# Optimization experiments

Measured on AMD Instinct MI355X. Metric: run time of the kernel, lower is better.

## Reference

```python
import jax, jax.numpy as jnp
import numpy as np

B, N, D = 4, 1024, 1024
H, DH = 16, 64            # heads, dim_head; inner_dim = H*DH = D
CTX_N, CTX_D = 77, 768    # CLIP text context
FF_IN, FF_HID = 8 * D, 4 * D  # GEGLU: proj to 2*4*D, gate to 4*D
EPS = 1e-5
SCALE = DH ** -0.5
NL = 256                  # 2**8 levels for all quantizers
ZP_QKV = 128.0            # asymmetric 8-bit zero point for q/k/v
ZP_W = 0.0                # always_zero=True for softmax-weight quantizer


def _round_ste(t):
    return t + jax.lax.stop_gradient(jnp.round(t) - t)


def _fake_quant(x, delta, zp):
    xq = jnp.clip(_round_ste(x / delta) + zp, 0.0, NL - 1.0)
    return (xq - zp) * delta


def _ln(x, w, b):
    m = x.mean(-1, keepdims=True)
    v = x.var(-1, keepdims=True)
    return (x - m) * jax.lax.rsqrt(v + EPS) * w + b


def _split_heads(t):  # [b, n, h*d] -> [b, h, n, d]
    b, n, _ = t.shape
    return t.reshape(b, n, H, DH).transpose(0, 2, 1, 3)


def _attn(x, ctx, wq, wk, wv, wo, bo, dq, dk, dv, dw):
    q = _split_heads(x @ wq)
    k = _split_heads(ctx @ wk)
    v = _split_heads(ctx @ wv)
    qq = _fake_quant(q, dq, ZP_QKV)
    kk = _fake_quant(k, dk, ZP_QKV)
    sim = jnp.einsum('bhid,bhjd->bhij', qq, kk) * SCALE
    attn = jax.nn.softmax(sim, axis=-1)
    aw = _fake_quant(attn, dw, ZP_W)
    vv = _fake_quant(v, dv, ZP_QKV)
    out = jnp.einsum('bhij,bhjd->bhid', aw, vv)
    b, _, n, _ = out.shape
    out = out.transpose(0, 2, 1, 3).reshape(b, n, H * DH)
    return out @ wo + bo


def _geglu_ff(x, w1, b1, w2, b2):
    h = x @ w1 + b1
    a, g = jnp.split(h, 2, axis=-1)
    return (a * jax.nn.gelu(g, approximate=False)) @ w2 + b2


def setup_inputs() -> dict:
    key = jax.random.key(0)
    ks = jax.random.split(key, 16)
    w = lambda i, shp, s: jax.random.normal(ks[i], shp, jnp.float32) * s
    sD = D ** -0.5
    sC = CTX_D ** -0.5
    return {
        'x': jax.random.normal(ks[0], (B, N, D), jnp.float32),
        'context': jax.random.normal(ks[1], (B, CTX_N, CTX_D), jnp.float32),
        'norm1_w': jnp.ones((D,), jnp.float32), 'norm1_b': jnp.zeros((D,), jnp.float32),
        'norm2_w': jnp.ones((D,), jnp.float32), 'norm2_b': jnp.zeros((D,), jnp.float32),
        'norm3_w': jnp.ones((D,), jnp.float32), 'norm3_b': jnp.zeros((D,), jnp.float32),
        'a1_wq': w(2, (D, D), sD), 'a1_wk': w(3, (D, D), sD), 'a1_wv': w(4, (D, D), sD),
        'a1_wo': w(5, (D, D), sD), 'a1_bo': jnp.zeros((D,), jnp.float32),
        'a2_wq': w(6, (D, D), sD), 'a2_wk': w(7, (CTX_D, D), sC), 'a2_wv': w(8, (CTX_D, D), sC),
        'a2_wo': w(9, (D, D), sD), 'a2_bo': jnp.zeros((D,), jnp.float32),
        'ff_w1': w(10, (D, FF_IN), sD), 'ff_b1': jnp.zeros((FF_IN,), jnp.float32),
        'ff_w2': w(11, (FF_HID, D), FF_HID ** -0.5), 'ff_b2': jnp.zeros((D,), jnp.float32),
        'd1_q': jnp.asarray(0.02, jnp.float32), 'd1_k': jnp.asarray(0.02, jnp.float32),
        'd1_v': jnp.asarray(0.02, jnp.float32), 'd1_w': jnp.asarray(1.0 / 255.0, jnp.float32),
        'd2_q': jnp.asarray(0.02, jnp.float32), 'd2_k': jnp.asarray(0.02, jnp.float32),
        'd2_v': jnp.asarray(0.02, jnp.float32), 'd2_w': jnp.asarray(1.0 / 255.0, jnp.float32),
    }


def reference(x, context, norm1_w, norm1_b, norm2_w, norm2_b, norm3_w, norm3_b,
              a1_wq, a1_wk, a1_wv, a1_wo, a1_bo,
              a2_wq, a2_wk, a2_wv, a2_wo, a2_bo,
              ff_w1, ff_b1, ff_w2, ff_b2,
              d1_q, d1_k, d1_v, d1_w, d2_q, d2_k, d2_v, d2_w):
    # attn1: quantized self-attention
    x = _attn(_ln(x, norm1_w, norm1_b), _ln(x, norm1_w, norm1_b),
              a1_wq, a1_wk, a1_wv, a1_wo, a1_bo, d1_q, d1_k, d1_v, d1_w) + x
    # attn2: quantized cross-attention with text context
    x = _attn(_ln(x, norm2_w, norm2_b), context,
              a2_wq, a2_wk, a2_wv, a2_wo, a2_bo, d2_q, d2_k, d2_v, d2_w) + x
    # GEGLU feed-forward
    x = _geglu_ff(_ln(x, norm3_w, norm3_b), ff_w1, ff_b1, ff_w2, ff_b2) + x
    return x
```

## Files before the change

kernel.cpp:

```cpp
#include <hip/hip_runtime.h>
#include <math.h>


typedef unsigned short u16;
typedef __attribute__((ext_vector_type(8))) short short8;
typedef __attribute__((ext_vector_type(4))) float f32x4;

__device__ inline float b2f(u16 v) { return __uint_as_float(((unsigned)v) << 16); }
__device__ inline u16 f2b(float f) {
  unsigned u = __float_as_uint(f);
  unsigned r = u + 0x7fffu + ((u >> 16) & 1u);
  return (u16)(r >> 16);
}

__device__ inline float exp2_fast(float x) {
#if __has_builtin(__builtin_amdgcn_exp2f)
  return __builtin_amdgcn_exp2f(x);
#else
  return __expf(x * 0.6931471805599453f);
#endif
}

__device__ inline void glds16(const u16* g, u16* l) {
  __builtin_amdgcn_global_load_lds(
      (const __attribute__((address_space(1))) void*)g,
      (__attribute__((address_space(3))) void*)l, 16, 0, 0);
}

__global__ __launch_bounds__(256) void transpose_k(const float* __restrict__ in,
                                                   u16* __restrict__ out,
                                                   int R, int C) {
  __shared__ float t[32][33];
  int tx = threadIdx.x & 31, ty = threadIdx.x >> 5;
  int c0 = blockIdx.x * 32, r0 = blockIdx.y * 32;
#pragma unroll
  for (int i = 0; i < 32; i += 8)
    t[ty + i][tx] = in[(size_t)(r0 + ty + i) * C + c0 + tx];
  __syncthreads();
#pragma unroll
  for (int i = 0; i < 32; i += 8)
    out[(size_t)(c0 + ty + i) * R + r0 + tx] = f2b(t[tx][ty + i]);
}

struct TrBatch { const float* in[4]; u16* out[4]; int R[4]; };
__global__ __launch_bounds__(256) void transpose4_k(TrBatch a) {
  int z = blockIdx.z;
  const float* in = a.in[z];
  u16* out = a.out[z];
  int R = a.R[z];
  int r0 = blockIdx.y * 32;
  if (r0 >= R) return;
  __shared__ float t[32][33];
  int tx = threadIdx.x & 31, ty = threadIdx.x >> 5;
  int c0 = blockIdx.x * 32;
#pragma unroll
  for (int i = 0; i < 32; i += 8)
    t[ty + i][tx] = in[(size_t)(r0 + ty + i) * 1024 + c0 + tx];
  __syncthreads();
#pragma unroll
  for (int i = 0; i < 32; i += 8)
    out[(size_t)(c0 + ty + i) * R + r0 + tx] = f2b(t[tx][ty + i]);
}

__global__ __launch_bounds__(256) void tr16_k(const u16* __restrict__ in,
                                              u16* __restrict__ out, int NK,
                                              int NKP) {
  __shared__ u16 t[32][33];
  int tx = threadIdx.x & 31, ty = threadIdx.x >> 5;
  int n0 = blockIdx.x * 32, c0 = blockIdx.y * 32, b = blockIdx.z;
  const u16* ib = in + (size_t)b * NK * 1024;
  u16* ob = out + (size_t)b * 1024 * NKP;
#pragma unroll
  for (int i = 0; i < 32; i += 8) {
    int n = n0 + ty + i;
    n = n < NK ? n : NK - 1;
    t[ty + i][tx] = ib[(size_t)n * 1024 + c0 + tx];
  }
  __syncthreads();
#pragma unroll
  for (int i = 0; i < 32; i += 8)
    ob[(size_t)(c0 + ty + i) * NKP + n0 + tx] = t[tx][ty + i];
}

__global__ __launch_bounds__(256) void cast_k(const float* __restrict__ in,
                                              u16* __restrict__ out) {
  int i = (blockIdx.x * 256 + threadIdx.x) * 4;
  float4 v = *(const float4*)(in + i);
  out[i + 0] = f2b(v.x);
  out[i + 1] = f2b(v.y);
  out[i + 2] = f2b(v.z);
  out[i + 3] = f2b(v.w);
}

__global__ __launch_bounds__(256) void zero_k(float4* __restrict__ out) {
  float4 z = {0.f, 0.f, 0.f, 0.f};
  out[blockIdx.x * 256 + threadIdx.x] = z;
}

__global__ __launch_bounds__(256) void ln_k(const float* __restrict__ X,
                                            const float* __restrict__ W,
                                            const float* __restrict__ Bi,
                                            u16* __restrict__ Out) {
  const int row = blockIdx.x, tid = threadIdx.x;
  float4 x = *(const float4*)(X + (size_t)row * 1024 + tid * 4);
  float s = x.x + x.y + x.z + x.w;
  float s2 = x.x * x.x + x.y * x.y + x.z * x.z + x.w * x.w;
#pragma unroll
  for (int off = 32; off >= 1; off >>= 1) {
    s += __shfl_down(s, off);
    s2 += __shfl_down(s2, off);
  }
  __shared__ float red[8];
  int wave = tid >> 6, lane = tid & 63;
  if (lane == 0) { red[wave] = s; red[4 + wave] = s2; }
  __syncthreads();
  s = red[0] + red[1] + red[2] + red[3];
  s2 = red[4] + red[5] + red[6] + red[7];
  float mean = s * 0.0009765625f;
  float var = s2 * 0.0009765625f - mean * mean;
  float rs = rsqrtf(var + 1e-5f);
  float4 w = *(const float4*)(W + tid * 4);
  float4 b = *(const float4*)(Bi + tid * 4);
  u16* orow = Out + (size_t)row * 1024 + tid * 4;
  orow[0] = f2b((x.x - mean) * rs * w.x + b.x);
  orow[1] = f2b((x.y - mean) * rs * w.y + b.y);
  orow[2] = f2b((x.z - mean) * rs * w.z + b.z);
  orow[3] = f2b((x.w - mean) * rs * w.w + b.w);
}

template <int EPI, int TM>
__global__ __launch_bounds__(256, 2) void gemm_bt(
    const u16* __restrict__ A, int lda, const u16* __restrict__ Bt, int ldb,
    void* __restrict__ Cp, int ldc, const float* __restrict__ bias,
    const float* __restrict__ res, int ldr, const float* __restrict__ dp,
    const float* __restrict__ dp2, const float* __restrict__ dp3,
    size_t segsz, int M, int N, int K) {
  __shared__ __align__(16) u16 As[TM * 64];
  __shared__ __align__(16) u16 Bs[128 * 64];
  const int tid = threadIdx.x;
  const int lane = tid & 63, wave = tid >> 6;
  const int qd = lane >> 4, cl = lane & 15;
  const int wm = (wave & 1) * (TM / 2), wn = (wave >> 1) << 6;
  const int m0 = blockIdx.x * TM, n0 = blockIdx.y * 128;

  f32x4 acc[TM / 32][4];
  const f32x4 zero = {0.f, 0.f, 0.f, 0.f};
#pragma unroll
  for (int i = 0; i < TM / 32; i++)
#pragma unroll
    for (int j = 0; j < 4; j++) acc[i][j] = zero;

  for (int k0 = 0; k0 < K; k0 += 64) {
    __syncthreads();
#pragma unroll
    for (int it = 0; it < TM / 32; ++it) {
      int ch = it * 256 + tid;
      int r = ch >> 3, cc = (ch & 7) << 3;
      int gr = m0 + r;
      gr = gr < M ? gr : M - 1;
      glds16(A + (size_t)gr * lda + k0 + cc, As + ch * 8);
    }
#pragma unroll
    for (int it = 0; it < 4; ++it) {
      int ch = it * 256 + tid;
      int r = ch >> 3, cc = (ch & 7) << 3;
      glds16(Bt + (size_t)(n0 + r) * ldb + k0 + cc, Bs + ch * 8);
    }
    __syncthreads();
#pragma unroll
    for (int ks = 0; ks < 64; ks += 32) {
      short8 af[TM / 32], bf[4];
#pragma unroll
      for (int t = 0; t < TM / 32; t++)
        af[t] = *(const short8*)(As + (wm + t * 16 + cl) * 64 + ks + qd * 8);
#pragma unroll
      for (int t = 0; t < 4; t++)
        bf[t] = *(const short8*)(Bs + (wn + t * 16 + cl) * 64 + ks + qd * 8);
#pragma unroll
      for (int mt = 0; mt < TM / 32; mt++)
#pragma unroll
        for (int nt = 0; nt < 4; nt++)
          acc[mt][nt] = __builtin_amdgcn_mfma_f32_16x16x32_bf16(
              af[mt], bf[nt], acc[mt][nt], 0, 0, 0);
    }
  }

  float dscale = 1.f;
  u16* qbase = (u16*)Cp;
  if constexpr (EPI == 0) dscale = 1.0f / dp[0];
  if constexpr (EPI == 2) {
    int seg = n0 >> 10;
    const float* ds = (seg == 0) ? dp : ((seg == 1) ? dp2 : dp3);
    dscale = 1.0f / ds[0];
    qbase = (u16*)Cp + (size_t)seg * segsz;
  }
#pragma unroll
  for (int mt = 0; mt < TM / 32; ++mt) {
#pragma unroll
    for (int r = 0; r < 4; ++r) {
      int row = m0 + wm + mt * 16 + qd * 4 + r;
      if (row >= M) continue;
#pragma unroll
      for (int nt = 0; nt < 4; ++nt) {
        int col = n0 + wn + nt * 16 + cl;
        float v = acc[mt][nt][r];
        if constexpr (EPI == 0) {
          float xq = rintf(v * dscale) + 128.f;
          xq = fminf(fmaxf(xq, 0.f), 255.f);
          qbase[(size_t)row * ldc + col] = f2b(xq - 128.f);
        } else if constexpr (EPI == 2) {
          float xq = rintf(v * dscale) + 128.f;
          xq = fminf(fmaxf(xq, 0.f), 255.f);
          qbase[(size_t)row * ldc + (col & 1023)] = f2b(xq - 128.f);
        } else {
          v += bias[col] + res[(size_t)row * ldr + col];
          ((float*)Cp)[(size_t)row * ldc + col] = v;
        }
      }
    }
  }
}

__global__ __launch_bounds__(256, 2) void gemm_bt_sk(
    const u16* __restrict__ A, int lda, const u16* __restrict__ Bt, int ldb,
    float* __restrict__ C, int ldc, const float* __restrict__ bias,
    const float* __restrict__ res, int ldr, int M, int KH) {
  __shared__ __align__(16) u16 As[128 * 64];
  __shared__ __align__(16) u16 Bs[128 * 64];
  const int tid = threadIdx.x;
  const int lane = tid & 63, wave = tid >> 6;
  const int qd = lane >> 4, cl = lane & 15;
  const int wm = (wave & 1) * 64, wn = (wave >> 1) << 6;
  const int m0 = blockIdx.x * 128, n0 = blockIdx.y * 128;
  const int kz = blockIdx.z;
  const int kbeg = kz * KH, kend = kbeg + KH;

  f32x4 acc[4][4];
  const f32x4 zero = {0.f, 0.f, 0.f, 0.f};
#pragma unroll
  for (int i = 0; i < 4; i++)
#pragma unroll
    for (int j = 0; j < 4; j++) acc[i][j] = zero;

  for (int k0 = kbeg; k0 < kend; k0 += 64) {
    __syncthreads();
#pragma unroll
    for (int it = 0; it < 4; ++it) {
      int ch = it * 256 + tid;
      int r = ch >> 3, cc = (ch & 7) << 3;
      glds16(A + (size_t)(m0 + r) * lda + k0 + cc, As + ch * 8);
    }
#pragma unroll
    for (int it = 0; it < 4; ++it) {
      int ch = it * 256 + tid;
      int r = ch >> 3, cc = (ch & 7) << 3;
      glds16(Bt + (size_t)(n0 + r) * ldb + k0 + cc, Bs + ch * 8);
    }
    __syncthreads();
#pragma unroll
    for (int ks = 0; ks < 64; ks += 32) {
      short8 af[4], bf[4];
#pragma unroll
      for (int t = 0; t < 4; t++)
        af[t] = *(const short8*)(As + (wm + t * 16 + cl) * 64 + ks + qd * 8);
#pragma unroll
      for (int t = 0; t < 4; t++)
        bf[t] = *(const short8*)(Bs + (wn + t * 16 + cl) * 64 + ks + qd * 8);
#pragma unroll
      for (int mt = 0; mt < 4; mt++)
#pragma unroll
        for (int nt = 0; nt < 4; nt++)
          acc[mt][nt] = __builtin_amdgcn_mfma_f32_16x16x32_bf16(
              af[mt], bf[nt], acc[mt][nt], 0, 0, 0);
    }
  }

#pragma unroll
  for (int mt = 0; mt < 4; ++mt) {
#pragma unroll
    for (int r = 0; r < 4; ++r) {
      int row = m0 + wm + mt * 16 + qd * 4 + r;
#pragma unroll
      for (int nt = 0; nt < 4; ++nt) {
        int col = n0 + wn + nt * 16 + cl;
        float v = acc[mt][nt][r];
        if (kz == 0) v += bias[col] + res[(size_t)row * ldr + col];
        atomicAdd(&C[(size_t)row * ldc + col], v);
      }
    }
  }
}

#define VMW(n) asm volatile("s_waitcnt vmcnt(" #n ")" ::: "memory")
#define LGKM0() asm volatile("s_waitcnt lgkmcnt(0)" ::: "memory")
#define SBAR() __builtin_amdgcn_s_barrier()
#define SCHED0() __builtin_amdgcn_sched_barrier(0)

#define ST_A(P, MH, K0)                                                      \
  do {                                                                       \
    _Pragma("unroll") for (int it = 0; it < 2; ++it) {                       \
      int r_ = (MH) * 128 + it * 64 + sr;                                    \
      glds16(Ag + (size_t)(m0 + r_) * 1024 + (K0) + ((sc ^ (r_ & 7)) << 3),  \
             As + (P) * 16384 + r_ * 64 + (sc << 3));                        \
    }                                                                        \
  } while (0)

#define ST_B(P, BH, K0)                                                      \
  do {                                                                       \
    _Pragma("unroll") for (int it = 0; it < 2; ++it) {                       \
      int r_ = it * 64 + sr;                                                 \
      glds16(W1t + (size_t)((BH) * 4096 + n0 + r_) * 1024 + (K0) +           \
                 ((sc ^ (r_ & 7)) << 3),                                     \
             Bs + (P) * 16384 + ((BH) * 128 + r_) * 64 + (sc << 3));         \
    }                                                                        \
  } while (0)

#define RDA(P, MH)                                                           \
  do {                                                                       \
    _Pragma("unroll") for (int mf = 0; mf < 4; ++mf) {                       \
      int row_ = (MH) * 128 + wr * 64 + mf * 16 + cl;                        \
      _Pragma("unroll") for (int ks = 0; ks < 2; ++ks)                       \
        af[mf * 2 + ks] = *(const short8*)(As + (P) * 16384 + row_ * 64 +    \
                                           (((ks * 4 + qd) ^ (cl & 7)) << 3)); \
    }                                                                        \
  } while (0)

#define RDB(P, NH, DST)                                                      \
  do {                                                                       \
    _Pragma("unroll") for (int nf = 0; nf < 2; ++nf) {                       \
      int j_ = (NH) * 128 + wc * 32 + nf * 16 + cl;                          \
      _Pragma("unroll") for (int ks = 0; ks < 2; ++ks)                       \
        DST[nf * 2 + ks] = *(const short8*)(Bs + (P) * 16384 + j_ * 64 +     \
                                            (((ks * 4 + qd) ^ (cl & 7)) << 3)); \
    }                                                                        \
  } while (0)

#define MFMAQ(MH, NH, BSET)                                                  \
  do {                                                                       \
    _Pragma("unroll") for (int mf = 0; mf < 4; ++mf)                         \
      _Pragma("unroll") for (int nf = 0; nf < 2; ++nf)                       \
        _Pragma("unroll") for (int ks = 0; ks < 2; ++ks)                     \
          acc[(MH) * 4 + mf][(NH) * 2 + nf] =                                \
              __builtin_amdgcn_mfma_f32_16x16x32_bf16(                       \
                  af[mf * 2 + ks], BSET[nf * 2 + ks],                        \
                  acc[(MH) * 4 + mf][(NH) * 2 + nf], 0, 0, 0);               \
  } while (0)

#define KTILE(P, KN, LAST)                                                   \
  do {                                                                       \
                            \
    RDA(P, 0);                                                               \
    RDB(P, 0, bU);                                                           \
    if (!(LAST)) ST_A((P) ^ 1, 0, KN);                                       \
    SBAR();                                                                  \
    LGKM0();                                                                 \
    SCHED0();                                                                \
    __builtin_amdgcn_s_setprio(1);                                           \
    MFMAQ(0, 0, bU);                                                         \
    __builtin_amdgcn_s_setprio(0);                                           \
    SCHED0();                                                                \
    if (LAST) { VMW(0); } else { VMW(2); }                                   \
    SBAR();                                                                  \
                                    \
    RDB(P, 1, bV);                                                           \
    if (!(LAST)) ST_B((P) ^ 1, 0, KN);                                       \
    SBAR();                                                                  \
    LGKM0();                                                                 \
    SCHED0();                                                                \
    __builtin_amdgcn_s_setprio(1);                                           \
    MFMAQ(0, 1, bV);                                                         \
    __builtin_amdgcn_s_setprio(0);                                           \
    SCHED0();                                                                \
    SBAR();                                                                  \
                                    \
    RDA(P, 1);                                                               \
    if (!(LAST)) ST_A((P) ^ 1, 1, KN);                                       \
    SBAR();                                                                  \
    LGKM0();                                                                 \
    SCHED0();                                                                \
    __builtin_amdgcn_s_setprio(1);                                           \
    MFMAQ(1, 1, bV);                                                         \
    __builtin_amdgcn_s_setprio(0);                                           \
    SCHED0();                                                                \
    SBAR();                                                                  \
                                       \
    if (!(LAST)) ST_B((P) ^ 1, 1, KN);                                       \
    SBAR();                                                                  \
    LGKM0();                                                                 \
    SCHED0();                                                                \
    __builtin_amdgcn_s_setprio(1);                                           \
    MFMAQ(1, 0, bU);                                                         \
    __builtin_amdgcn_s_setprio(0);                                           \
    SCHED0();                                                                \
    if (!(LAST)) VMW(4);                                                     \
    SBAR();                                                                  \
  } while (0)

__global__ __launch_bounds__(512, 1) void ff1_geglu8_k(
    const u16* __restrict__ Ag, const u16* __restrict__ W1t,
    const float* __restrict__ b1, u16* __restrict__ gg) {
  __shared__ __align__(16) u16 smem[65536];
  u16* As = smem;
  u16* Bs = smem + 32768;
  const int tid = threadIdx.x;
  const int lane = tid & 63, wave = tid >> 6;
  const int qd = lane >> 4, cl = lane & 15;
  const int wr = wave >> 2, wc = wave & 3;
  const int m0 = blockIdx.x * 256;
  const int n0 = blockIdx.y * 128;
  const int sr = tid >> 3, sc = tid & 7;

  f32x4 acc[8][4];
  const f32x4 zero = {0.f, 0.f, 0.f, 0.f};
#pragma unroll
  for (int i = 0; i < 8; ++i)
#pragma unroll
    for (int j = 0; j < 4; ++j) acc[i][j] = zero;
  short8 af[8], bU[4], bV[4];

  ST_A(0, 0, 0);
  ST_B(0, 0, 0);
  ST_A(0, 1, 0);
  ST_B(0, 1, 0);
  VMW(0);
  SBAR();
  SCHED0();

  int p = 0;
#pragma unroll 1
  for (int t = 0; t < 15; ++t) {
    KTILE(p, (t + 1) * 64, 0);
    p ^= 1;
  }
  KTILE(1, 0, 1);

#pragma unroll
  for (int i = 0; i < 8; ++i) {
    const int row = m0 + (i >> 2) * 128 + wr * 64 + (i & 3) * 16 + qd * 4;
#pragma unroll
    for (int nf = 0; nf < 2; ++nf) {
      const int col = n0 + wc * 32 + nf * 16 + cl;
      const float ba = b1[col];
      const float bg = b1[4096 + col];
#pragma unroll
      for (int r = 0; r < 4; ++r) {
        float a = acc[i][nf][r] + ba;
        float g = acc[i][2 + nf][r] + bg;
        float ge = 0.5f * g * (1.0f + erff(g * 0.70710678118654752f));
        gg[(size_t)(row + r) * 4096 + col] = f2b(a * ge);
      }
    }
  }
}

__global__ __launch_bounds__(256, 4) void attn_k(
    const u16* __restrict__ Q, const u16* __restrict__ Kb,
    const u16* __restrict__ VbT, u16* __restrict__ O,
    const float* dqp, const float* dkp, const float* dvp, const float* dwp,
    int NK, int NKP) {
  __shared__ __align__(16) u16 Ks[64 * 64];
  __shared__ __align__(16) u16 VTs[64 * 64];
  __shared__ __align__(16) u16 Ps[4][16 * 72];
  const int tid = threadIdx.x;
  const int lane = tid & 63, wave = tid >> 6;
  const int qd = lane >> 4, cl = lane & 15;
  const int b = blockIdx.z, h = blockIdx.y, qt = blockIdx.x;
  const float ss2 = dqp[0] * dkp[0] * 0.125f * 1.4426950408889634f;
  const float oscale = dwp[0] * dvp[0];
  const float inv_dw = 1.0f / dwp[0];
  const f32x4 zero = {0.f, 0.f, 0.f, 0.f};

  short8 qf0, qf1;
  {
    const u16* qrow =
        Q + (size_t)(b * 1024 + qt * 64 + wave * 16 + cl) * 1024 + h * 64;
    qf0 = *(const short8*)(qrow + qd * 8);
    qf1 = *(const short8*)(qrow + 32 + qd * 8);
  }

  const u16* kbase = Kb + (size_t)(b * NK) * 1024 + h * 64;
  const u16* vtbase = VbT + ((size_t)b * 1024 + h * 64) * NKP;
  const int r_st = tid >> 3;
  const int c_sw = (((tid & 7) ^ (r_st & 7)) << 3);

  float m_s = -1e30f, l_s = 0.f;
  for (int j0 = 0; j0 < NK; j0 += 64) {
    __syncthreads();
#pragma unroll
    for (int it = 0; it < 2; ++it) {
      int j = j0 + it * 32 + r_st;
      j = j < NK ? j : NK - 1;
      glds16(kbase + (size_t)j * 1024 + c_sw, Ks + (it * 256 + tid) * 8);
    }
    __syncthreads();
    const bool full = (j0 + 64 <= NK);
    float sc[16];
#pragma unroll
    for (int nt = 0; nt < 4; ++nt) {
      const int row = nt * 16 + cl, sw = cl & 7;
      short8 kf0 = *(const short8*)(Ks + row * 64 + ((qd ^ sw) << 3));
      short8 kf1 = *(const short8*)(Ks + row * 64 + (((4 | qd) ^ sw) << 3));
      f32x4 st = zero;
      st = __builtin_amdgcn_mfma_f32_16x16x32_bf16(kf0, qf0, st, 0, 0, 0);
      st = __builtin_amdgcn_mfma_f32_16x16x32_bf16(kf1, qf1, st, 0, 0, 0);
#pragma unroll
      for (int r = 0; r < 4; ++r) {
        int key = j0 + nt * 16 + qd * 4 + r;
        sc[nt * 4 + r] = (full || key < NK) ? st[r] * ss2 : -1e30f;
      }
    }
    float t0 = fmaxf(fmaxf(sc[0], sc[1]), sc[2]);
    float t1 = fmaxf(fmaxf(sc[3], sc[4]), sc[5]);
    float t2 = fmaxf(fmaxf(sc[6], sc[7]), sc[8]);
    float t3 = fmaxf(fmaxf(sc[9], sc[10]), sc[11]);
    float t4 = fmaxf(fmaxf(sc[12], sc[13]), sc[14]);
    float mx = fmaxf(fmaxf(fmaxf(t0, t1), fmaxf(t2, t3)), fmaxf(t4, sc[15]));
    mx = fmaxf(mx, __shfl_xor(mx, 16));
    mx = fmaxf(mx, __shfl_xor(mx, 32));
    float mn = fmaxf(m_s, mx);
    float ss = 0.f;
#pragma unroll
    for (int i = 0; i < 16; ++i) ss += exp2_fast(sc[i] - mn);
    ss += __shfl_xor(ss, 16);
    ss += __shfl_xor(ss, 32);
    l_s = l_s * exp2_fast(m_s - mn) + ss;
    m_s = mn;
  }
  const float mb = m_s + log2f(l_s) - log2f(inv_dw);

  f32x4 oacc[4];
#pragma unroll
  for (int t = 0; t < 4; t++) oacc[t] = zero;

  for (int j0 = 0; j0 < NK; j0 += 64) {
    __syncthreads();
#pragma unroll
    for (int it = 0; it < 2; ++it) {
      int r = it * 32 + r_st;
      int j = j0 + r;
      j = j < NK ? j : NK - 1;
      glds16(kbase + (size_t)j * 1024 + c_sw, Ks + (it * 256 + tid) * 8);
      glds16(vtbase + (size_t)r * NKP + j0 + c_sw, VTs + (it * 256 + tid) * 8);
    }
    __syncthreads();
    const bool full = (j0 + 64 <= NK);
#pragma unroll
    for (int nt = 0; nt < 4; ++nt) {
      const int row = nt * 16 + cl, sw = cl & 7;
      short8 kf0 = *(const short8*)(Ks + row * 64 + ((qd ^ sw) << 3));
      short8 kf1 = *(const short8*)(Ks + row * 64 + (((4 | qd) ^ sw) << 3));
      f32x4 st = zero;
      st = __builtin_amdgcn_mfma_f32_16x16x32_bf16(kf0, qf0, st, 0, 0, 0);
      st = __builtin_amdgcn_mfma_f32_16x16x32_bf16(kf1, qf1, st, 0, 0, 0);
      unsigned a[4];
#pragma unroll
      for (int r = 0; r < 4; ++r) {
        int key = j0 + nt * 16 + qd * 4 + r;
        float aw = 0.f;
        if (full || key < NK) {
          float e = exp2_fast(__builtin_fmaf(st[r], ss2, -mb));
          aw = fminf(rintf(e), 255.f);
        }
        a[r] = __float_as_uint(aw);
      }
      uint2 pv;
      pv.x = (a[0] >> 16) | (a[1] & 0xffff0000u);
      pv.y = (a[2] >> 16) | (a[3] & 0xffff0000u);
      *(uint2*)(&Ps[wave][cl * 72 + nt * 16 + qd * 4]) = pv;
    }
#pragma unroll
    for (int ks = 0; ks < 2; ++ks) {
      short8 pf = *(const short8*)(&Ps[wave][cl * 72 + ks * 32 + qd * 8]);
#pragma unroll
      for (int dt = 0; dt < 4; ++dt) {
        const int vrow = dt * 16 + cl;
        short8 vf = *(const short8*)(VTs + vrow * 64 +
                                     (((ks * 4 + qd) ^ (cl & 7)) << 3));
        oacc[dt] = __builtin_amdgcn_mfma_f32_16x16x32_bf16(pf, vf, oacc[dt],
                                                           0, 0, 0);
      }
    }
  }
#pragma unroll
  for (int dt = 0; dt < 4; ++dt)
#pragma unroll
    for (int r = 0; r < 4; r++) {
      size_t addr =
          (size_t)(b * 1024 + qt * 64 + wave * 16 + qd * 4 + r) * 1024 +
          h * 64 + dt * 16 + cl;
      O[addr] = f2b(oacc[dt][r] * oscale);
    }
}

extern "C" void kernel_launch(void* const* d_in, const int* in_sizes, int n_in,
                              void* d_out, int out_size, void* d_ws,
                              size_t ws_size, hipStream_t stream) {
  (void)in_sizes; (void)n_in; (void)out_size; (void)ws_size;
  const float* x    = (const float*)d_in[0];
  const float* ctx  = (const float*)d_in[1];
  const float* n1w  = (const float*)d_in[2];
  const float* n1b  = (const float*)d_in[3];
  const float* n2w  = (const float*)d_in[4];
  const float* n2b  = (const float*)d_in[5];
  const float* n3w  = (const float*)d_in[6];
  const float* n3b  = (const float*)d_in[7];
  const float* a1wq = (const float*)d_in[8];
  const float* a1wk = (const float*)d_in[9];
  const float* a1wv = (const float*)d_in[10];
  const float* a1wo = (const float*)d_in[11];
  const float* a1bo = (const float*)d_in[12];
  const float* a2wq = (const float*)d_in[13];
  const float* a2wk = (const float*)d_in[14];
  const float* a2wv = (const float*)d_in[15];
  const float* a2wo = (const float*)d_in[16];
  const float* a2bo = (const float*)d_in[17];
  const float* ffw1 = (const float*)d_in[18];
  const float* ffb1 = (const float*)d_in[19];
  const float* ffw2 = (const float*)d_in[20];
  const float* ffb2 = (const float*)d_in[21];
  const float* d1q = (const float*)d_in[22];
  const float* d1k = (const float*)d_in[23];
  const float* d1v = (const float*)d_in[24];
  const float* d1w = (const float*)d_in[25];
  const float* d2q = (const float*)d_in[26];
  const float* d2k = (const float*)d_in[27];
  const float* d2v = (const float*)d_in[28];
  const float* d2w = (const float*)d_in[29];

  char* ws = (char*)d_ws;
  const size_t MB = 1u << 20;
  u16* W    = (u16*)(ws + 0 * MB);
  u16* lnb  = (u16*)(ws + 16 * MB);
  u16* qb   = (u16*)(ws + 24 * MB);
  u16* kb   = (u16*)(ws + 32 * MB);
  u16* vb   = (u16*)(ws + 40 * MB);
  u16* vbT  = (u16*)(ws + 48 * MB);
  u16* ao   = (u16*)(ws + 56 * MB);
  float* x1 = (float*)(ws + 64 * MB);
  u16* k2b  = (u16*)(ws + 32 * MB);
  u16* v2b  = k2b + 308 * 1024;
  u16* vbTc = (u16*)(ws + 34 * MB);
  u16* ctxb = (u16*)(ws + 35 * MB);
  u16* gg   = (u16*)(ws + 24 * MB);

  u16* WT0 = W;
  u16* WT1 = (u16*)(ws + 2 * MB);
  u16* WT2 = (u16*)(ws + 4 * MB);
  u16* WT3 = (u16*)(ws + 6 * MB);
  u16* WT3c = WT2 + 1024 * 768;

  dim3 T256(256);
  {
    TrBatch tb;
    tb.in[0] = a1wq; tb.out[0] = WT0; tb.R[0] = 1024;
    tb.in[1] = a1wk; tb.out[1] = WT1; tb.R[1] = 1024;
    tb.in[2] = a1wv; tb.out[2] = WT2; tb.R[2] = 1024;
    tb.in[3] = a1wo; tb.out[3] = WT3; tb.R[3] = 1024;
    transpose4_k<<<dim3(32, 32, 4), T256, 0, stream>>>(tb);
  }
  ln_k<<<4096, T256, 0, stream>>>(x, n1w, n1b, lnb);
  gemm_bt<2, 128><<<dim3(32, 24), T256, 0, stream>>>(
      lnb, 1024, WT0, 1024, qb, 1024, nullptr, nullptr, 0, d1q, d1k, d1v,
      (size_t)4096 * 1024, 4096, 3072, 1024);
  tr16_k<<<dim3(32, 32, 4), T256, 0, stream>>>(vb, vbT, 1024, 1024);
  attn_k<<<dim3(16, 16, 4), T256, 0, stream>>>(qb, kb, vbT, ao, d1q, d1k, d1v,
                                               d1w, 1024, 1024);
  gemm_bt<1, 64><<<dim3(64, 8), T256, 0, stream>>>(
      ao, 1024, WT3, 1024, x1, 1024, a1bo, x, 1024, nullptr, nullptr, nullptr,
      0, 4096, 1024, 1024);
  {
    TrBatch tb;
    tb.in[0] = a2wq; tb.out[0] = WT0; tb.R[0] = 1024;
    tb.in[1] = a2wo; tb.out[1] = WT1; tb.R[1] = 1024;
    tb.in[2] = a2wk; tb.out[2] = WT2;  tb.R[2] = 768;
    tb.in[3] = a2wv; tb.out[3] = WT3c; tb.R[3] = 768;
    transpose4_k<<<dim3(32, 32, 4), T256, 0, stream>>>(tb);
  }
  ln_k<<<4096, T256, 0, stream>>>(x1, n2w, n2b, lnb);
  cast_k<<<231, T256, 0, stream>>>(ctx, ctxb);
  gemm_bt<0, 64><<<dim3(64, 8), T256, 0, stream>>>(
      lnb, 1024, WT0, 1024, qb, 1024, nullptr, nullptr, 0, d2q, nullptr,
      nullptr, 0, 4096, 1024, 1024);
  gemm_bt<2, 64><<<dim3(5, 16), T256, 0, stream>>>(
      ctxb, 768, WT2, 768, k2b, 1024, nullptr, nullptr, 0, d2k, d2v, nullptr,
      (size_t)308 * 1024, 308, 2048, 768);
  tr16_k<<<dim3(3, 32, 4), T256, 0, stream>>>(v2b, vbTc, 77, 128);
  attn_k<<<dim3(16, 16, 4), T256, 0, stream>>>(qb, k2b, vbTc, ao, d2q, d2k,
                                               d2v, d2w, 77, 128);
  gemm_bt<1, 64><<<dim3(64, 8), T256, 0, stream>>>(
      ao, 1024, WT1, 1024, x1, 1024, a2bo, x1, 1024, nullptr, nullptr, nullptr,
      0, 4096, 1024, 1024);
  transpose_k<<<dim3(256, 32), T256, 0, stream>>>(ffw1, W, 1024, 8192);
  ln_k<<<4096, T256, 0, stream>>>(x1, n3w, n3b, lnb);
  ff1_geglu8_k<<<dim3(16, 32), dim3(512), 0, stream>>>(lnb, W, ffb1, gg);
  transpose_k<<<dim3(32, 128), T256, 0, stream>>>(ffw2, W, 4096, 1024);
  zero_k<<<4096, T256, 0, stream>>>((float4*)d_out);
  gemm_bt_sk<<<dim3(32, 8, 2), T256, 0, stream>>>(
      gg, 4096, W, 4096, (float*)d_out, 1024, ffb2, x1, 1024, 4096, 2048);
}
```

Measured before the change: 557.0 us.

## Use 512-thread 128x128 GEMM for out-projections and FF2, drop split-K atomics

Adds a templated gemm512 kernel with 8 waves per 128x128 tile (each wave computes 64x32) and swaps it in for the two attention output projections, the cross-attention Q projection, and the FF2 GEMM. For FF2 it replaces the split-K kernel, its atomicAdd epilogue and the zero-fill launch with a single full-K pass that writes results directly. The intent is fewer launches, no atomics, and larger tiles with more waves to hide latency. The cost is fewer blocks (256) for the 1024-wide GEMMs, which may underfill the GPU, and a longer serial K loop for FF2.

```diff
diff --git a/kernel.cpp b/kernel.cpp
--- a/kernel.cpp
+++ b/kernel.cpp
@@ -90,11 +90,6 @@
   out[i + 1] = f2b(v.y);
   out[i + 2] = f2b(v.z);
   out[i + 3] = f2b(v.w);
-}
-
-__global__ __launch_bounds__(256) void zero_k(float4* __restrict__ out) {
-  float4 z = {0.f, 0.f, 0.f, 0.f};
-  out[blockIdx.x * 256 + threadIdx.x] = z;
 }
 
 __global__ __launch_bounds__(256) void ln_k(const float* __restrict__ X,
@@ -221,71 +216,79 @@
   }
 }
 
-__global__ __launch_bounds__(256, 2) void gemm_bt_sk(
+template <int EPI>
+__global__ __launch_bounds__(512, 1) void gemm512(
     const u16* __restrict__ A, int lda, const u16* __restrict__ Bt, int ldb,
-    float* __restrict__ C, int ldc, const float* __restrict__ bias,
-    const float* __restrict__ res, int ldr, int M, int KH) {
+    void* __restrict__ Cp, int ldc, const float* __restrict__ bias,
+    const float* __restrict__ res, int ldr, const float* __restrict__ dp,
+    int K) {
   __shared__ __align__(16) u16 As[128 * 64];
   __shared__ __align__(16) u16 Bs[128 * 64];
   const int tid = threadIdx.x;
   const int lane = tid & 63, wave = tid >> 6;
   const int qd = lane >> 4, cl = lane & 15;
-  const int wm = (wave & 1) * 64, wn = (wave >> 1) << 6;
+  const int wm = (wave >> 2) << 6, wn = (wave & 3) << 5;
   const int m0 = blockIdx.x * 128, n0 = blockIdx.y * 128;
-  const int kz = blockIdx.z;
-  const int kbeg = kz * KH, kend = kbeg + KH;
-
-  f32x4 acc[4][4];
+
+  f32x4 acc[4][2];
   const f32x4 zero = {0.f, 0.f, 0.f, 0.f};
 #pragma unroll
   for (int i = 0; i < 4; i++)
 #pragma unroll
-    for (int j = 0; j < 4; j++) acc[i][j] = zero;
-
-  for (int k0 = kbeg; k0 < kend; k0 += 64) {
-    __syncthreads();
-#pragma unroll
-    for (int it = 0; it < 4; ++it) {
-      int ch = it * 256 + tid;
+    for (int j = 0; j < 2; j++) acc[i][j] = zero;
+
+  for (int k0 = 0; k0 < K; k0 += 64) {
+    __syncthreads();
+#pragma unroll
+    for (int it = 0; it < 2; ++it) {
+      int ch = it * 512 + tid;
       int r = ch >> 3, cc = (ch & 7) << 3;
       glds16(A + (size_t)(m0 + r) * lda + k0 + cc, As + ch * 8);
     }
 #pragma unroll
-    for (int it = 0; it < 4; ++it) {
-      int ch = it * 256 + tid;
+    for (int it = 0; it < 2; ++it) {
+      int ch = it * 512 + tid;
       int r = ch >> 3, cc = (ch & 7) << 3;
       glds16(Bt + (size_t)(n0 + r) * ldb + k0 + cc, Bs + ch * 8);
     }
     __syncthreads();
 #pragma unroll
     for (int ks = 0; ks < 64; ks += 32) {
-      short8 af[4], bf[4];
+      short8 af[4], bf[2];
 #pragma unroll
       for (int t = 0; t < 4; t++)
         af[t] = *(const short8*)(As + (wm + t * 16 + cl) * 64 + ks + qd * 8);
 #pragma unroll
-      for (int t = 0; t < 4; t++)
+      for (int t = 0; t < 2; t++)
         bf[t] = *(const short8*)(Bs + (wn + t * 16 + cl) * 64 + ks + qd * 8);
 #pragma unroll
       for (int mt = 0; mt < 4; mt++)
 #pragma unroll
-        for (int nt = 0; nt < 4; nt++)
+        for (int nt = 0; nt < 2; nt++)
           acc[mt][nt] = __builtin_amdgcn_mfma_f32_16x16x32_bf16(
               af[mt], bf[nt], acc[mt][nt], 0, 0, 0);
     }
   }
 
+  float dscale = 1.f;
+  if constexpr (EPI == 0) dscale = 1.0f / dp[0];
 #pragma unroll
   for (int mt = 0; mt < 4; ++mt) {
 #pragma unroll
     for (int r = 0; r < 4; ++r) {
       int row = m0 + wm + mt * 16 + qd * 4 + r;
 #pragma unroll
-      for (int nt = 0; nt < 4; ++nt) {
+      for (int nt = 0; nt < 2; ++nt) {
         int col = n0 + wn + nt * 16 + cl;
         float v = acc[mt][nt][r];
-        if (kz == 0) v += bias[col] + res[(size_t)row * ldr + col];
-        atomicAdd(&C[(size_t)row * ldc + col], v);
+        if constexpr (EPI == 0) {
+          float xq = rintf(v * dscale) + 128.f;
+          xq = fminf(fmaxf(xq, 0.f), 255.f);
+          ((u16*)Cp)[(size_t)row * ldc + col] = f2b(xq - 128.f);
+        } else {
+          v += bias[col] + res[(size_t)row * ldr + col];
+          ((float*)Cp)[(size_t)row * ldc + col] = v;
+        }
       }
     }
   }
@@ -665,9 +668,8 @@
   tr16_k<<<dim3(32, 32, 4), T256, 0, stream>>>(vb, vbT, 1024, 1024);
   attn_k<<<dim3(16, 16, 4), T256, 0, stream>>>(qb, kb, vbT, ao, d1q, d1k, d1v,
                                                d1w, 1024, 1024);
-  gemm_bt<1, 64><<<dim3(64, 8), T256, 0, stream>>>(
-      ao, 1024, WT3, 1024, x1, 1024, a1bo, x, 1024, nullptr, nullptr, nullptr,
-      0, 4096, 1024, 1024);
+  gemm512<1><<<dim3(32, 8), dim3(512), 0, stream>>>(
+      ao, 1024, WT3, 1024, x1, 1024, a1bo, x, 1024, nullptr, 1024);
   {
     TrBatch tb;
     tb.in[0] = a2wq; tb.out[0] = WT0; tb.R[0] = 1024;
@@ -678,23 +680,20 @@
   }
   ln_k<<<4096, T256, 0, stream>>>(x1, n2w, n2b, lnb);
   cast_k<<<231, T256, 0, stream>>>(ctx, ctxb);
-  gemm_bt<0, 64><<<dim3(64, 8), T256, 0, stream>>>(
-      lnb, 1024, WT0, 1024, qb, 1024, nullptr, nullptr, 0, d2q, nullptr,
-      nullptr, 0, 4096, 1024, 1024);
+  gemm512<0><<<dim3(32, 8), dim3(512), 0, stream>>>(
+      lnb, 1024, WT0, 1024, qb, 1024, nullptr, nullptr, 0, d2q, 1024);
   gemm_bt<2, 64><<<dim3(5, 16), T256, 0, stream>>>(
       ctxb, 768, WT2, 768, k2b, 1024, nullptr, nullptr, 0, d2k, d2v, nullptr,
       (size_t)308 * 1024, 308, 2048, 768);
   tr16_k<<<dim3(3, 32, 4), T256, 0, stream>>>(v2b, vbTc, 77, 128);
   attn_k<<<dim3(16, 16, 4), T256, 0, stream>>>(qb, k2b, vbTc, ao, d2q, d2k,
                                                d2v, d2w, 77, 128);
-  gemm_bt<1, 64><<<dim3(64, 8), T256, 0, stream>>>(
-      ao, 1024, WT1, 1024, x1, 1024, a2bo, x1, 1024, nullptr, nullptr, nullptr,
-      0, 4096, 1024, 1024);
+  gemm512<1><<<dim3(32, 8), dim3(512), 0, stream>>>(
+      ao, 1024, WT1, 1024, x1, 1024, a2bo, x1, 1024, nullptr, 1024);
   transpose_k<<<dim3(256, 32), T256, 0, stream>>>(ffw1, W, 1024, 8192);
   ln_k<<<4096, T256, 0, stream>>>(x1, n3w, n3b, lnb);
   ff1_geglu8_k<<<dim3(16, 32), dim3(512), 0, stream>>>(lnb, W, ffb1, gg);
   transpose_k<<<dim3(32, 128), T256, 0, stream>>>(ffw2, W, 4096, 1024);
-  zero_k<<<4096, T256, 0, stream>>>((float4*)d_out);
-  gemm_bt_sk<<<dim3(32, 8, 2), T256, 0, stream>>>(
-      gg, 4096, W, 4096, (float*)d_out, 1024, ffb2, x1, 1024, 4096, 2048);
-}
+  gemm512<1><<<dim3(32, 8), dim3(512), 0, stream>>>(
+      gg, 4096, W, 4096, d_out, 1024, ffb2, x1, 1024, nullptr, 4096);
+}
```

Result: slower. 573.0 us (+2.9%).
